# Optimization experiments

Measured on AMD Instinct MI355X. Metric: run time of the kernel, lower is better.

The kernel has to match this reference:

```python
import jax, jax.numpy as jnp
import numpy as np

INNER_DIM = 512
SCALE = 1.0 / np.sqrt(INNER_DIM).astype(np.float32)  # module scales by 1/sqrt(inner_dim), not head_dim


def setup_inputs() -> dict:
    key = jax.random.key(0)
    ks = jax.random.split(key, 7)
    b, n, d = 4, 4096, 512
    s = 0.02
    return {
        "x": jax.random.normal(ks[0], (b, n, d), jnp.float32),
        "y": jax.random.normal(ks[1], (b, n, d), jnp.float32),
        "Wq": jax.random.normal(ks[2], (INNER_DIM, d), jnp.float32) * s,  # torch Linear weight [out, in]
        "Wk": jax.random.normal(ks[3], (INNER_DIM, d), jnp.float32) * s,
        "Wv": jax.random.normal(ks[4], (INNER_DIM, d), jnp.float32) * s,
        "Wo": jax.random.normal(ks[5], (d, INNER_DIM), jnp.float32) * s,
        "bo": jax.random.normal(ks[6], (d,), jnp.float32) * s,
    }


def reference(x, y, Wq, Wk, Wv, Wo, bo):
    # q, k from x; v from y (bias-free projections)
    q = jnp.einsum('bnd,id->bni', x, Wq)
    k = jnp.einsum('bnd,id->bni', x, Wk)
    v = jnp.einsum('bnd,id->bni', y, Wv)
    # full [b, n, n] scores, scaled by 1/sqrt(inner_dim)
    alpha = jnp.einsum('bik,bjk->bij', q, k) * SCALE
    alpha = jax.nn.softmax(alpha, axis=-1)
    ctx = jnp.einsum('bij,bjd->bid', alpha, v)
    out = jnp.einsum('bid,od->bio', ctx, Wo) + bo
    return out
```

## Files before the change

kernel.cpp:

```cpp
#include <hip/hip_runtime.h>
#include <hip/hip_bf16.h>


typedef unsigned short u16;
typedef __bf16 bf16x8 __attribute__((ext_vector_type(8)));
typedef float f32x4 __attribute__((ext_vector_type(4)));

#define SCALE_QK 0.044194173824159216f

__device__ __forceinline__ u16 f2bf(float f) {
    __hip_bfloat16 h = __float2bfloat16(f);
    return __builtin_bit_cast(u16, h);
}

__device__ __forceinline__ void load_lds16(const void* g, void* l) {
    __builtin_amdgcn_global_load_lds(
        (const __attribute__((address_space(1))) void*)g,
        (__attribute__((address_space(3))) void*)l, 16, 0, 0);
}

__global__ void cvt_bf16_kernel(const float* __restrict__ src, u16* __restrict__ dst,
                                int n8, float scale) {
    int i = blockIdx.x * blockDim.x + threadIdx.x;
    if (i >= n8) return;
    const float4* s4 = (const float4*)src;
    float4 v0 = s4[2 * i], v1 = s4[2 * i + 1];
    union { u16 u[8]; uint4 v; } o;
    o.u[0] = f2bf(v0.x * scale); o.u[1] = f2bf(v0.y * scale);
    o.u[2] = f2bf(v0.z * scale); o.u[3] = f2bf(v0.w * scale);
    o.u[4] = f2bf(v1.x * scale); o.u[5] = f2bf(v1.y * scale);
    o.u[6] = f2bf(v1.z * scale); o.u[7] = f2bf(v1.w * scale);
    ((uint4*)dst)[i] = o.v;
}

__global__ void wvo_kernel(const float* __restrict__ Wo, const float* __restrict__ Wv,
                           float* __restrict__ Wvo) {
    int o = blockIdx.x, t = threadIdx.x;
    float a0 = 0.f, a1 = 0.f;
    for (int i = 0; i < 512; ++i) {
        float w = Wo[o * 512 + i];
        a0 += w * Wv[i * 512 + t];
        a1 += w * Wv[i * 512 + t + 256];
    }
    Wvo[o * 512 + t] = a0;
    Wvo[o * 512 + t + 256] = a1;
}

__launch_bounds__(512, 2)
__global__ void gemm256_exp_kernel(const u16* __restrict__ A, const u16* __restrict__ B,
                                   u16* __restrict__ Cout, int N, int lda, int ldb,
                                   long long sAz, long long sBz, long long sCz) {
    __shared__ u16 lds[8][8192];

    const int tid = threadIdx.x;
    const int wave = tid >> 6, lane = tid & 63;
    const int lr = lane & 15, lg = lane >> 4;
    const int wm = wave >> 2, wn = wave & 3;

    int bid = (blockIdx.z * gridDim.y + blockIdx.y) * gridDim.x + blockIdx.x;
    int lgc = (bid & 7) * 128 + (bid >> 3);
    const int bx = lgc & 15;
    int rem = lgc >> 4;
    const int by = rem & 15, z = rem >> 4;
    const int row0 = by * 256, col0 = bx * 256;

    const u16* Ab = A + (size_t)z * sAz;
    const u16* Bb = B + (size_t)z * sBz;

    const int rb = lane >> 2;
    const int kg8 = ((lane & 3) ^ (rb & 3)) << 3;

    f32x4 acc[8][4];
#pragma unroll
    for (int i = 0; i < 8; ++i)
#pragma unroll
        for (int j = 0; j < 4; ++j) acc[i][j] = (f32x4){0.f, 0.f, 0.f, 0.f};

#define STAGE_HALF(s_, slot_)                                                     \
    {                                                                             \
        const int h_ = (s_)&3, ts_ = (s_) >> 2;                                   \
        const u16* G_ = (h_ & 1) ? Bb : Ab;                                       \
        const int pan_ = (h_ & 1) ? col0 : row0;                                  \
        const int ld_ = (h_ & 1) ? ldb : lda;                                     \
        const int kofs_ = ts_ * 64 + (h_ >> 1) * 32 + kg8;                        \
        _Pragma("unroll") for (int j_ = 0; j_ < 2; ++j_) {                        \
            int r_ = (j_ * 8 + wave) * 16 + rb;                                   \
            load_lds16(G_ + (size_t)(pan_ + r_) * ld_ + kofs_,                    \
                       &lds[slot_][(j_ * 8 + wave) * 512]);                       \
        }                                                                         \
    }

    #pragma unroll
    for (int s = 0; s < 6; ++s) STAGE_HALF(s, s);
    asm volatile("s_waitcnt vmcnt(4)");
    __builtin_amdgcn_sched_barrier(0);
    __builtin_amdgcn_s_barrier();

    bf16x8 bfr[4];

#pragma unroll
    for (int i = 0; i < 4; ++i) {
#pragma unroll
        for (int p = 0; p < 8; ++p) {
            const int q = p & 3;
            const int ks = q >> 1;
            const int aslot = (p >> 2) * 4 + 2 * ks;
            const int bslot = aslot + 1;
            const int fmb = (q & 1) * 4;

            bf16x8 af[4];
#pragma unroll
            for (int f = 0; f < 4; ++f) {
                int row = wm * 128 + (fmb + f) * 16 + lr;
                af[f] = *(const bf16x8*)&lds[aslot][row * 32 + ((lg ^ (lr & 3)) << 3)];
            }
            if (q == 0 || q == 2) {
#pragma unroll
                for (int f = 0; f < 4; ++f) {
                    int row = wn * 64 + f * 16 + lr;
                    bfr[f] = *(const bf16x8*)&lds[bslot][row * 32 + ((lg ^ (lr & 3)) << 3)];
                }
            }

            {
                const int s = 8 * i + p + 6;
                if (s < 32) {
                    const int slot = (p + 6) & 7;
                    STAGE_HALF(s, slot);
                }
            }

            __builtin_amdgcn_sched_barrier(0);
            __builtin_amdgcn_s_barrier();
            asm volatile("s_waitcnt lgkmcnt(0)");
            __builtin_amdgcn_sched_barrier(0);

            __builtin_amdgcn_s_setprio(1);
#pragma unroll
            for (int f = 0; f < 4; ++f)
#pragma unroll
                for (int n = 0; n < 4; ++n)
                    acc[fmb + f][n] = __builtin_amdgcn_mfma_f32_16x16x32_bf16(
                        af[f], bfr[n], acc[fmb + f][n], 0, 0, 0);
            __builtin_amdgcn_s_setprio(0);

            if (p == 3) {
                if (i == 3) asm volatile("s_waitcnt vmcnt(0)");
                else        asm volatile("s_waitcnt vmcnt(4)");
            } else if (p == 7 && i < 3) {
                asm volatile("s_waitcnt vmcnt(4)");
            }
            __builtin_amdgcn_sched_barrier(0);
            __builtin_amdgcn_s_barrier();
        }
    }
#undef STAGE_HALF

    u16* C = Cout + (size_t)z * sCz;
#pragma unroll
    for (int fm = 0; fm < 8; ++fm)
#pragma unroll
        for (int fn = 0; fn < 4; ++fn)
#pragma unroll
            for (int reg = 0; reg < 4; ++reg) {
                int r = row0 + wm * 128 + fm * 16 + lg * 4 + reg;
                int c = col0 + wn * 64 + fn * 16 + lr;
                C[(size_t)r * N + c] = f2bf(__expf(acc[fm][fn][reg]));
            }
}

template <int EPI>
__launch_bounds__(256)
__global__ void gemm_bt_kernel(const u16* __restrict__ A, const u16* __restrict__ B,
                               void* __restrict__ Cout, int N, int K, int lda, int ldb,
                               long long sAz, long long sBz, long long sCz) {
    __shared__ u16 As[2][128 * 32];
    __shared__ u16 Bs[2][128 * 32];

    const int tid = threadIdx.x;
    const int wave = tid >> 6, lane = tid & 63;
    const int lr = lane & 15, lg = lane >> 4;
    const int wr = wave >> 1, wc = wave & 1;

    const int gx = gridDim.x, gy = gridDim.y;
    int bid = (blockIdx.z * gy + blockIdx.y) * gx + blockIdx.x;
    const int nwg = gx * gy * gridDim.z;
    int lgc = (bid & 7) * (nwg >> 3) + (bid >> 3);
    const int bx = lgc % gx;
    int rem = lgc / gx;
    const int by = rem % gy, z = rem / gy;
    const int row0 = by * 128, col0 = bx * 128;

    const u16* Ab = A + (size_t)z * sAz;
    const u16* Bb = B + (size_t)z * sBz;

    f32x4 acc[4][4];
#pragma unroll
    for (int i = 0; i < 4; ++i)
#pragma unroll
        for (int j = 0; j < 4; ++j) acc[i][j] = (f32x4){0.f, 0.f, 0.f, 0.f};

    const int KT = K >> 5;

#define STAGE(bufi, kt2)                                                          \
    {                                                                             \
        _Pragma("unroll") for (int i = 0; i < 2; ++i) {                           \
            int chunk = i * 256 + tid;                                            \
            int r = chunk >> 2, c4 = chunk & 3;                                   \
            load_lds16(Ab + (size_t)(row0 + r) * lda + (kt2) * 32 + c4 * 8,       \
                       &As[bufi][(i * 256 + wave * 64) * 8]);                     \
            load_lds16(Bb + (size_t)(col0 + r) * ldb + (kt2) * 32 + c4 * 8,       \
                       &Bs[bufi][(i * 256 + wave * 64) * 8]);                     \
        }                                                                         \
    }

    STAGE(0, 0);
    int buf = 0;
    for (int kt = 0; kt < KT; ++kt) {
        __syncthreads();
        if (kt + 1 < KT) STAGE(buf ^ 1, kt + 1);

        bf16x8 af[4], bfr[4];
#pragma unroll
        for (int mf = 0; mf < 4; ++mf)
            af[mf] = *(const bf16x8*)&As[buf][(wr * 64 + mf * 16 + lr) * 32 + lg * 8];
#pragma unroll
        for (int nf = 0; nf < 4; ++nf)
            bfr[nf] = *(const bf16x8*)&Bs[buf][(wc * 64 + nf * 16 + lr) * 32 + lg * 8];
#pragma unroll
        for (int mf = 0; mf < 4; ++mf)
#pragma unroll
            for (int nf = 0; nf < 4; ++nf)
                acc[mf][nf] = __builtin_amdgcn_mfma_f32_16x16x32_bf16(
                    af[mf], bfr[nf], acc[mf][nf], 0, 0, 0);
        buf ^= 1;
    }
#undef STAGE

    const int rbase = row0 + wr * 64;
    const int cbase = col0 + wc * 64;

    if (EPI == 0) {
        u16* C = (u16*)Cout + (size_t)z * sCz;
#pragma unroll
        for (int mf = 0; mf < 4; ++mf)
#pragma unroll
            for (int nf = 0; nf < 4; ++nf)
#pragma unroll
                for (int reg = 0; reg < 4; ++reg) {
                    int r = rbase + mf * 16 + lg * 4 + reg;
                    int c = cbase + nf * 16 + lr;
                    C[(size_t)r * N + c] = f2bf(acc[mf][nf][reg]);
                }
    } else {
        u16* C = (u16*)Cout;
#pragma unroll
        for (int mf = 0; mf < 4; ++mf)
#pragma unroll
            for (int nf = 0; nf < 4; ++nf) {
                int rg = rbase + mf * 16 + lg * 4;
                int bsel = rg >> 12, rl = rg & 4095;
                int c = cbase + nf * 16 + lr;
                union { u16 u[4]; uint2 v; } o;
#pragma unroll
                for (int reg = 0; reg < 4; ++reg) o.u[reg] = f2bf(acc[mf][nf][reg]);
                *(uint2*)(C + ((size_t)bsel << 21) + ((size_t)c << 12) + rl) = o.v;
            }
    }
}

__launch_bounds__(512, 4)
__global__ void pv_kernel(const u16* __restrict__ P, const u16* __restrict__ vwT,
                          float* __restrict__ part, float* __restrict__ lpart) {
    __shared__ u16 As[2][64 * 32];
    __shared__ u16 Bs[2][512 * 32];

    const int tid = threadIdx.x;
    const int wave = tid >> 6, lane = tid & 63;
    const int lr = lane & 15, lg = lane >> 4;

    int bid = blockIdx.x;
    int lgc = (bid & 7) * 64 + (bid >> 3);
    const int rp = lgc & 63;
    const int ks = (lgc >> 6) & 1;
    const int z = lgc >> 7;
    const int row0 = rp * 64;

    const u16* Pz = P + (size_t)z * 16777216 + (size_t)row0 * 4096 + ks * 2048;
    const u16* Vz = vwT + (size_t)z * 2097152 + ks * 2048;

    f32x4 acc[4][4];
#pragma unroll
    for (int i = 0; i < 4; ++i)
#pragma unroll
        for (int j = 0; j < 4; ++j) acc[i][j] = (f32x4){0.f, 0.f, 0.f, 0.f};
    float rs = 0.f;

#define STAGE(bufi, kt2)                                                          \
    {                                                                             \
        if (tid < 256) {                                                          \
            int r = tid >> 2, c4 = tid & 3;                                       \
            load_lds16(Pz + (size_t)r * 4096 + (kt2) * 32 + c4 * 8,               \
                       &As[bufi][wave * 512]);                                    \
        }                                                                         \
        _Pragma("unroll") for (int it = 0; it < 4; ++it) {                        \
            int c = it * 512 + tid;                                               \
            int r = c >> 2, c4 = c & 3;                                           \
            load_lds16(Vz + (size_t)r * 4096 + (kt2) * 32 + c4 * 8,               \
                       &Bs[bufi][(it * 512 + wave * 64) * 8]);                    \
        }                                                                         \
    }

    STAGE(0, 0);
    int buf = 0;
    for (int kt = 0; kt < 64; ++kt) {
        __syncthreads();
        if (kt + 1 < 64) STAGE(buf ^ 1, kt + 1);

        {
            uint2 rv = *(const uint2*)&As[buf][(tid >> 3) * 32 + (tid & 7) * 4];
            rs += __uint_as_float(rv.x << 16) + __uint_as_float(rv.x & 0xffff0000u) +
                  __uint_as_float(rv.y << 16) + __uint_as_float(rv.y & 0xffff0000u);
        }

        bf16x8 af[4];
#pragma unroll
        for (int mf = 0; mf < 4; ++mf)
            af[mf] = *(const bf16x8*)&As[buf][(mf * 16 + lr) * 32 + lg * 8];
#pragma unroll
        for (int nf = 0; nf < 4; ++nf) {
            bf16x8 bfr = *(const bf16x8*)&Bs[buf][(wave * 64 + nf * 16 + lr) * 32 + lg * 8];
#pragma unroll
            for (int mf = 0; mf < 4; ++mf)
                acc[mf][nf] = __builtin_amdgcn_mfma_f32_16x16x32_bf16(
                    af[mf], bfr, acc[mf][nf], 0, 0, 0);
        }
        buf ^= 1;
    }
#undef STAGE

    rs += __shfl_xor(rs, 1, 64);
    rs += __shfl_xor(rs, 2, 64);
    rs += __shfl_xor(rs, 4, 64);
    if ((tid & 7) == 0)
        lpart[(size_t)ks * 16384 + z * 4096 + row0 + (tid >> 3)] = rs;

    float* O = part + (size_t)ks * 8388608 + ((size_t)z * 4096 + row0) * 512;
#pragma unroll
    for (int mf = 0; mf < 4; ++mf)
#pragma unroll
        for (int nf = 0; nf < 4; ++nf) {
            int c = wave * 64 + nf * 16 + lr;
#pragma unroll
            for (int reg = 0; reg < 4; ++reg) {
                int r = mf * 16 + lg * 4 + reg;
                O[(size_t)r * 512 + c] = acc[mf][nf][reg];
            }
        }
}

__global__ void reduce_kernel(const float* __restrict__ part,
                              const float* __restrict__ lpart,
                              const float* __restrict__ bo,
                              float* __restrict__ out) {
    int i = blockIdx.x * blockDim.x + threadIdx.x;
    int r = i >> 7, c4 = i & 127;
    float inv = 1.0f / (lpart[r] + lpart[16384 + r]);
    float4 a = ((const float4*)part)[i];
    float4 b = ((const float4*)part)[i + 2097152];
    float4 bi = ((const float4*)bo)[c4];
    float4 o;
    o.x = (a.x + b.x) * inv + bi.x;
    o.y = (a.y + b.y) * inv + bi.y;
    o.z = (a.z + b.z) * inv + bi.z;
    o.w = (a.w + b.w) * inv + bi.w;
    ((float4*)out)[i] = o;
}

extern "C" void kernel_launch(void* const* d_in, const int* in_sizes, int n_in,
                              void* d_out, int out_size, void* d_ws, size_t ws_size,
                              hipStream_t stream) {
    const float* x  = (const float*)d_in[0];
    const float* y  = (const float*)d_in[1];
    const float* Wq = (const float*)d_in[2];
    const float* Wk = (const float*)d_in[3];
    const float* Wv = (const float*)d_in[4];
    const float* Wo = (const float*)d_in[5];
    const float* bo = (const float*)d_in[6];
    float* out = (float*)d_out;

    char* ws = (char*)d_ws;
    u16*   xb   = (u16*)(ws + 0);
    u16*   yb   = (u16*)(ws + 16777216);
    u16*   qk   = (u16*)(ws + 33554432);
    float* part = (float*)(ws + 0);
    u16*   vwT  = (u16*)(ws + 67108864);
    u16*   Wqkb = (u16*)(ws + 83886080);
    u16*   Wvob = (u16*)(ws + 84934656);
    float* Wvo  = (float*)(ws + 85458944);
    float* lpart= (float*)(ws + 86507520);
    u16*   P    = (u16*)(ws + 86638592);

    cvt_bf16_kernel<<<4096, 256, 0, stream>>>(x, xb, 1048576, 1.0f);
    cvt_bf16_kernel<<<4096, 256, 0, stream>>>(y, yb, 1048576, 1.0f);
    cvt_bf16_kernel<<<128, 256, 0, stream>>>(Wq, Wqkb, 32768, SCALE_QK);
    cvt_bf16_kernel<<<128, 256, 0, stream>>>(Wk, Wqkb + 262144, 32768, 1.0f);

    wvo_kernel<<<512, 256, 0, stream>>>(Wo, Wv, Wvo);
    cvt_bf16_kernel<<<128, 256, 0, stream>>>(Wvo, Wvob, 32768, 1.0f);

    gemm_bt_kernel<0><<<dim3(8, 128, 1), 256, 0, stream>>>(xb, Wqkb, qk,
                                                           1024, 512, 512, 512, 0, 0, 0);
    gemm_bt_kernel<1><<<dim3(4, 128, 1), 256, 0, stream>>>(yb, Wvob, vwT,
                                                           512, 512, 512, 512, 0, 0, 0);

    gemm256_exp_kernel<<<dim3(16, 16, 4), 512, 0, stream>>>(qk, qk + 512, P,
                                                            4096, 1024, 1024,
                                                            4194304, 4194304, 16777216);

    pv_kernel<<<512, 512, 0, stream>>>(P, vwT, part, lpart);

    reduce_kernel<<<8192, 256, 0, stream>>>(part, lpart, bo, out);
}
```

Measured before the change: 315.8 us.

## Retile PV GEMM to 256x256 pipeline, fuse fp32 conversion into projections

Replaces the 64-row PV kernel with a 256x256-tile kernel that uses a deep 8-slot LDS pipeline with swizzled layout, mirroring the QK kernel, so V tiles are reused across more rows. The projection GEMMs now read fp32 x/y directly and convert to bf16 in registers, which removes two full-size conversion passes. wvo_kernel computes four output rows per block so each Wv load is reused. The larger tiles reduce redundant global traffic but give fewer blocks and put more pressure on registers.

Result: slower. 334.2 us (+5.8%).

```diff
diff --git a/kernel.cpp b/kernel.cpp
--- a/kernel.cpp
+++ b/kernel.cpp
@@ -35,15 +35,22 @@
 
 __global__ void wvo_kernel(const float* __restrict__ Wo, const float* __restrict__ Wv,
                            float* __restrict__ Wvo) {
-    int o = blockIdx.x, t = threadIdx.x;
-    float a0 = 0.f, a1 = 0.f;
+    int ob = blockIdx.x * 4, t = threadIdx.x;
+    float a[4][2] = {{0.f, 0.f}, {0.f, 0.f}, {0.f, 0.f}, {0.f, 0.f}};
     for (int i = 0; i < 512; ++i) {
-        float w = Wo[o * 512 + i];
-        a0 += w * Wv[i * 512 + t];
-        a1 += w * Wv[i * 512 + t + 256];
-    }
-    Wvo[o * 512 + t] = a0;
-    Wvo[o * 512 + t + 256] = a1;
+        float v0 = Wv[i * 512 + t], v1 = Wv[i * 512 + t + 256];
+#pragma unroll
+        for (int r = 0; r < 4; ++r) {
+            float w = Wo[(ob + r) * 512 + i];
+            a[r][0] += w * v0;
+            a[r][1] += w * v1;
+        }
+    }
+#pragma unroll
+    for (int r = 0; r < 4; ++r) {
+        Wvo[(ob + r) * 512 + t] = a[r][0];
+        Wvo[(ob + r) * 512 + t + 256] = a[r][1];
+    }
 }
 
 __launch_bounds__(512, 2)
@@ -169,11 +176,158 @@
             }
 }
 
+__launch_bounds__(512, 2)
+__global__ void pv8_kernel(const u16* __restrict__ P, const u16* __restrict__ vwT,
+                           float* __restrict__ part, float* __restrict__ lpart) {
+    __shared__ u16 lds[8][8192];
+
+    const int tid = threadIdx.x;
+    const int wave = tid >> 6, lane = tid & 63;
+    const int lr = lane & 15, lg = lane >> 4;
+    const int wm = wave >> 2, wn = wave & 3;
+
+    int bid = blockIdx.x;
+    int lgc = (bid & 7) * 32 + (bid >> 3);
+    const int rp = lgc & 15;
+    const int t5 = lgc >> 4;
+    const int cx = t5 & 1, ks = (t5 >> 1) & 1, z = t5 >> 2;
+    const int row0 = rp * 256;
+    const int col0 = cx * 256;
+
+    const u16* Ab = P + (size_t)z * 16777216 + (size_t)ks * 2048;
+    const u16* Bb = vwT + (size_t)z * 2097152 + (size_t)ks * 2048;
+
+    const int rb = lane >> 2;
+    const int kg8 = ((lane & 3) ^ (rb & 3)) << 3;
+
+    f32x4 acc[8][4];
+#pragma unroll
+    for (int i = 0; i < 8; ++i)
+#pragma unroll
+        for (int j = 0; j < 4; ++j) acc[i][j] = (f32x4){0.f, 0.f, 0.f, 0.f};
+    float rsm[8] = {0.f, 0.f, 0.f, 0.f, 0.f, 0.f, 0.f, 0.f};
+
+#define STAGE_HALF(s_, slot_)                                                     \
+    {                                                                             \
+        const int h_ = (s_)&3, ts_ = (s_) >> 2;                                   \
+        const u16* G_ = (h_ & 1) ? Bb : Ab;                                       \
+        const int pan_ = (h_ & 1) ? col0 : row0;                                  \
+        const int kofs_ = ts_ * 64 + (h_ >> 1) * 32 + kg8;                        \
+        _Pragma("unroll") for (int j_ = 0; j_ < 2; ++j_) {                        \
+            int r_ = (j_ * 8 + wave) * 16 + rb;                                   \
+            load_lds16(G_ + (size_t)(pan_ + r_) * 4096 + kofs_,                   \
+                       &lds[slot_][(j_ * 8 + wave) * 512]);                       \
+        }                                                                         \
+    }
+
+    #pragma unroll
+    for (int s = 0; s < 6; ++s) STAGE_HALF(s, s);
+    asm volatile("s_waitcnt vmcnt(4)");
+    __builtin_amdgcn_sched_barrier(0);
+    __builtin_amdgcn_s_barrier();
+
+    bf16x8 bfr[4];
+
+    for (int i = 0; i < 16; ++i) {
+#pragma unroll
+        for (int p = 0; p < 8; ++p) {
+            const int q = p & 3;
+            const int ksl = q >> 1;
+            const int aslot = (p >> 2) * 4 + 2 * ksl;
+            const int bslot = aslot + 1;
+            const int fmb = (q & 1) * 4;
+
+            bf16x8 af[4];
+#pragma unroll
+            for (int f = 0; f < 4; ++f) {
+                int row = wm * 128 + (fmb + f) * 16 + lr;
+                af[f] = *(const bf16x8*)&lds[aslot][row * 32 + ((lg ^ (lr & 3)) << 3)];
+            }
+            if (q == 0 || q == 2) {
+#pragma unroll
+                for (int f = 0; f < 4; ++f) {
+                    int row = wn * 64 + f * 16 + lr;
+                    bfr[f] = *(const bf16x8*)&lds[bslot][row * 32 + ((lg ^ (lr & 3)) << 3)];
+                }
+            }
+
+            {
+                const int s = 8 * i + p + 6;
+                if (s < 128) {
+                    const int slot = (p + 6) & 7;
+                    STAGE_HALF(s, slot);
+                }
+            }
+
+            __builtin_amdgcn_sched_barrier(0);
+            __builtin_amdgcn_s_barrier();
+            asm volatile("s_waitcnt lgkmcnt(0)");
+            __builtin_amdgcn_sched_barrier(0);
+
+            __builtin_amdgcn_s_setprio(1);
+#pragma unroll
+            for (int f = 0; f < 4; ++f)
+#pragma unroll
+                for (int n = 0; n < 4; ++n)
+                    acc[fmb + f][n] = __builtin_amdgcn_mfma_f32_16x16x32_bf16(
+                        af[f], bfr[n], acc[fmb + f][n], 0, 0, 0);
+            __builtin_amdgcn_s_setprio(0);
+
+            if (wn == 0) {
+#pragma unroll
+                for (int f = 0; f < 4; ++f) {
+                    union { bf16x8 v; unsigned u[4]; } cv;
+                    cv.v = af[f];
+#pragma unroll
+                    for (int w = 0; w < 4; ++w)
+                        rsm[fmb + f] += __uint_as_float(cv.u[w] << 16) +
+                                        __uint_as_float(cv.u[w] & 0xffff0000u);
+                }
+            }
+
+            if (p == 3) {
+                if (i == 15) asm volatile("s_waitcnt vmcnt(0)");
+                else         asm volatile("s_waitcnt vmcnt(4)");
+            } else if (p == 7 && i < 15) {
+                asm volatile("s_waitcnt vmcnt(4)");
+            }
+            __builtin_amdgcn_sched_barrier(0);
+            __builtin_amdgcn_s_barrier();
+        }
+    }
+#undef STAGE_HALF
+
+    if (wn == 0) {
+#pragma unroll
+        for (int j = 0; j < 8; ++j) {
+            rsm[j] += __shfl_xor(rsm[j], 16, 64);
+            rsm[j] += __shfl_xor(rsm[j], 32, 64);
+        }
+        if (cx == 0 && lg == 0) {
+            float* lp = lpart + (size_t)ks * 16384 + z * 4096 + row0 + wm * 128;
+#pragma unroll
+            for (int j = 0; j < 8; ++j) lp[j * 16 + lr] = rsm[j];
+        }
+    }
+
+    float* O = part + (size_t)ks * 8388608 + ((size_t)z * 4096 + row0) * 512;
+#pragma unroll
+    for (int fm = 0; fm < 8; ++fm)
+#pragma unroll
+        for (int fn = 0; fn < 4; ++fn) {
+            int c = col0 + wn * 64 + fn * 16 + lr;
+#pragma unroll
+            for (int reg = 0; reg < 4; ++reg) {
+                int r = wm * 128 + fm * 16 + lg * 4 + reg;
+                O[(size_t)r * 512 + c] = acc[fm][fn][reg];
+            }
+        }
+}
+
 template <int EPI>
 __launch_bounds__(256)
-__global__ void gemm_bt_kernel(const u16* __restrict__ A, const u16* __restrict__ B,
-                               void* __restrict__ Cout, int N, int K, int lda, int ldb,
-                               long long sAz, long long sBz, long long sCz) {
+__global__ void gemm_f32a_kernel(const float* __restrict__ A, const u16* __restrict__ B,
+                                 void* __restrict__ Cout, int N, int K, int lda, int ldb) {
     __shared__ u16 As[2][128 * 32];
     __shared__ u16 Bs[2][128 * 32];
 
@@ -183,17 +337,12 @@
     const int wr = wave >> 1, wc = wave & 1;
 
     const int gx = gridDim.x, gy = gridDim.y;
-    int bid = (blockIdx.z * gy + blockIdx.y) * gx + blockIdx.x;
-    const int nwg = gx * gy * gridDim.z;
+    int bid = blockIdx.y * gx + blockIdx.x;
+    const int nwg = gx * gy;
     int lgc = (bid & 7) * (nwg >> 3) + (bid >> 3);
-    const int bx = lgc % gx;
-    int rem = lgc / gx;
-    const int by = rem % gy, z = rem / gy;
+    const int bx = lgc % gx, by = lgc / gx;
     const int row0 = by * 128, col0 = bx * 128;
 
-    const u16* Ab = A + (size_t)z * sAz;
-    const u16* Bb = B + (size_t)z * sBz;
-
     f32x4 acc[4][4];
 #pragma unroll
     for (int i = 0; i < 4; ++i)
@@ -201,24 +350,50 @@
         for (int j = 0; j < 4; ++j) acc[i][j] = (f32x4){0.f, 0.f, 0.f, 0.f};
 
     const int KT = K >> 5;
-
-#define STAGE(bufi, kt2)                                                          \
+    float4 ar[2][2];
+
+#define LOADA(kt2)                                                                \
     {                                                                             \
         _Pragma("unroll") for (int i = 0; i < 2; ++i) {                           \
             int chunk = i * 256 + tid;                                            \
             int r = chunk >> 2, c4 = chunk & 3;                                   \
-            load_lds16(Ab + (size_t)(row0 + r) * lda + (kt2) * 32 + c4 * 8,       \
-                       &As[bufi][(i * 256 + wave * 64) * 8]);                     \
-            load_lds16(Bb + (size_t)(col0 + r) * ldb + (kt2) * 32 + c4 * 8,       \
+            const float* src = A + (size_t)(row0 + r) * lda + (kt2) * 32 + c4 * 8;\
+            ar[i][0] = *(const float4*)src;                                       \
+            ar[i][1] = *(const float4*)(src + 4);                                 \
+        }                                                                         \
+    }
+#define WRITEA(bufi)                                                              \
+    {                                                                             \
+        _Pragma("unroll") for (int i = 0; i < 2; ++i) {                           \
+            int chunk = i * 256 + tid;                                            \
+            union { u16 u[8]; uint4 v; } cv;                                      \
+            const float* f = (const float*)&ar[i][0];                             \
+            _Pragma("unroll") for (int j = 0; j < 8; ++j) cv.u[j] = f2bf(f[j]);   \
+            *(uint4*)&As[bufi][chunk * 8] = cv.v;                                 \
+        }                                                                         \
+    }
+#define STAGEB(bufi, kt2)                                                         \
+    {                                                                             \
+        _Pragma("unroll") for (int i = 0; i < 2; ++i) {                           \
+            int chunk = i * 256 + tid;                                            \
+            int r = chunk >> 2, c4 = chunk & 3;                                   \
+            load_lds16(B + (size_t)(col0 + r) * ldb + (kt2) * 32 + c4 * 8,        \
                        &Bs[bufi][(i * 256 + wave * 64) * 8]);                     \
         }                                                                         \
     }
 
-    STAGE(0, 0);
+    LOADA(0);
+    WRITEA(0);
+    LOADA(1);
+    STAGEB(0, 0);
     int buf = 0;
     for (int kt = 0; kt < KT; ++kt) {
         __syncthreads();
-        if (kt + 1 < KT) STAGE(buf ^ 1, kt + 1);
+        if (kt + 1 < KT) {
+            WRITEA(buf ^ 1);
+            STAGEB(buf ^ 1, kt + 1);
+        }
+        if (kt + 2 < KT) LOADA(kt + 2);
 
         bf16x8 af[4], bfr[4];
 #pragma unroll
@@ -235,13 +410,15 @@
                     af[mf], bfr[nf], acc[mf][nf], 0, 0, 0);
         buf ^= 1;
     }
-#undef STAGE
+#undef LOADA
+#undef WRITEA
+#undef STAGEB
 
     const int rbase = row0 + wr * 64;
     const int cbase = col0 + wc * 64;
 
     if (EPI == 0) {
-        u16* C = (u16*)Cout + (size_t)z * sCz;
+        u16* C = (u16*)Cout;
 #pragma unroll
         for (int mf = 0; mf < 4; ++mf)
 #pragma unroll
@@ -267,96 +444,6 @@
                 *(uint2*)(C + ((size_t)bsel << 21) + ((size_t)c << 12) + rl) = o.v;
             }
     }
-}
-
-__launch_bounds__(512, 4)
-__global__ void pv_kernel(const u16* __restrict__ P, const u16* __restrict__ vwT,
-                          float* __restrict__ part, float* __restrict__ lpart) {
-    __shared__ u16 As[2][64 * 32];
-    __shared__ u16 Bs[2][512 * 32];
-
-    const int tid = threadIdx.x;
-    const int wave = tid >> 6, lane = tid & 63;
-    const int lr = lane & 15, lg = lane >> 4;
-
-    int bid = blockIdx.x;
-    int lgc = (bid & 7) * 64 + (bid >> 3);
-    const int rp = lgc & 63;
-    const int ks = (lgc >> 6) & 1;
-    const int z = lgc >> 7;
-    const int row0 = rp * 64;
-
-    const u16* Pz = P + (size_t)z * 16777216 + (size_t)row0 * 4096 + ks * 2048;
-    const u16* Vz = vwT + (size_t)z * 2097152 + ks * 2048;
-
-    f32x4 acc[4][4];
-#pragma unroll
-    for (int i = 0; i < 4; ++i)
-#pragma unroll
-        for (int j = 0; j < 4; ++j) acc[i][j] = (f32x4){0.f, 0.f, 0.f, 0.f};
-    float rs = 0.f;
-
-#define STAGE(bufi, kt2)                                                          \
-    {                                                                             \
-        if (tid < 256) {                                                          \
-            int r = tid >> 2, c4 = tid & 3;                                       \
-            load_lds16(Pz + (size_t)r * 4096 + (kt2) * 32 + c4 * 8,               \
-                       &As[bufi][wave * 512]);                                    \
-        }                                                                         \
-        _Pragma("unroll") for (int it = 0; it < 4; ++it) {                        \
-            int c = it * 512 + tid;                                               \
-            int r = c >> 2, c4 = c & 3;                                           \
-            load_lds16(Vz + (size_t)r * 4096 + (kt2) * 32 + c4 * 8,               \
-                       &Bs[bufi][(it * 512 + wave * 64) * 8]);                    \
-        }                                                                         \
-    }
-
-    STAGE(0, 0);
-    int buf = 0;
-    for (int kt = 0; kt < 64; ++kt) {
-        __syncthreads();
-        if (kt + 1 < 64) STAGE(buf ^ 1, kt + 1);
-
-        {
-            uint2 rv = *(const uint2*)&As[buf][(tid >> 3) * 32 + (tid & 7) * 4];
-            rs += __uint_as_float(rv.x << 16) + __uint_as_float(rv.x & 0xffff0000u) +
-                  __uint_as_float(rv.y << 16) + __uint_as_float(rv.y & 0xffff0000u);
-        }
-
-        bf16x8 af[4];
-#pragma unroll
-        for (int mf = 0; mf < 4; ++mf)
-            af[mf] = *(const bf16x8*)&As[buf][(mf * 16 + lr) * 32 + lg * 8];
-#pragma unroll
-        for (int nf = 0; nf < 4; ++nf) {
-            bf16x8 bfr = *(const bf16x8*)&Bs[buf][(wave * 64 + nf * 16 + lr) * 32 + lg * 8];
-#pragma unroll
-            for (int mf = 0; mf < 4; ++mf)
-                acc[mf][nf] = __builtin_amdgcn_mfma_f32_16x16x32_bf16(
-                    af[mf], bfr, acc[mf][nf], 0, 0, 0);
-        }
-        buf ^= 1;
-    }
-#undef STAGE
-
-    rs += __shfl_xor(rs, 1, 64);
-    rs += __shfl_xor(rs, 2, 64);
-    rs += __shfl_xor(rs, 4, 64);
-    if ((tid & 7) == 0)
-        lpart[(size_t)ks * 16384 + z * 4096 + row0 + (tid >> 3)] = rs;
-
-    float* O = part + (size_t)ks * 8388608 + ((size_t)z * 4096 + row0) * 512;
-#pragma unroll
-    for (int mf = 0; mf < 4; ++mf)
-#pragma unroll
-        for (int nf = 0; nf < 4; ++nf) {
-            int c = wave * 64 + nf * 16 + lr;
-#pragma unroll
-            for (int reg = 0; reg < 4; ++reg) {
-                int r = mf * 16 + lg * 4 + reg;
-                O[(size_t)r * 512 + c] = acc[mf][nf][reg];
-            }
-        }
 }
 
 __global__ void reduce_kernel(const float* __restrict__ part,
@@ -390,9 +477,7 @@
     float* out = (float*)d_out;
 
     char* ws = (char*)d_ws;
-    u16*   xb   = (u16*)(ws + 0);
-    u16*   yb   = (u16*)(ws + 16777216);
-    u16*   qk   = (u16*)(ws + 33554432);
+    u16*   qk   = (u16*)(ws + 0);
     float* part = (float*)(ws + 0);
     u16*   vwT  = (u16*)(ws + 67108864);
     u16*   Wqkb = (u16*)(ws + 83886080);
@@ -401,24 +486,19 @@
     float* lpart= (float*)(ws + 86507520);
     u16*   P    = (u16*)(ws + 86638592);
 
-    cvt_bf16_kernel<<<4096, 256, 0, stream>>>(x, xb, 1048576, 1.0f);
-    cvt_bf16_kernel<<<4096, 256, 0, stream>>>(y, yb, 1048576, 1.0f);
     cvt_bf16_kernel<<<128, 256, 0, stream>>>(Wq, Wqkb, 32768, SCALE_QK);
     cvt_bf16_kernel<<<128, 256, 0, stream>>>(Wk, Wqkb + 262144, 32768, 1.0f);
-
-    wvo_kernel<<<512, 256, 0, stream>>>(Wo, Wv, Wvo);
+    wvo_kernel<<<128, 256, 0, stream>>>(Wo, Wv, Wvo);
     cvt_bf16_kernel<<<128, 256, 0, stream>>>(Wvo, Wvob, 32768, 1.0f);
 
-    gemm_bt_kernel<0><<<dim3(8, 128, 1), 256, 0, stream>>>(xb, Wqkb, qk,
-                                                           1024, 512, 512, 512, 0, 0, 0);
-    gemm_bt_kernel<1><<<dim3(4, 128, 1), 256, 0, stream>>>(yb, Wvob, vwT,
-                                                           512, 512, 512, 512, 0, 0, 0);
+    gemm_f32a_kernel<0><<<dim3(8, 128), 256, 0, stream>>>(x, Wqkb, qk, 1024, 512, 512, 512);
+    gemm_f32a_kernel<1><<<dim3(4, 128), 256, 0, stream>>>(y, Wvob, vwT, 512, 512, 512, 512);
 
     gemm256_exp_kernel<<<dim3(16, 16, 4), 512, 0, stream>>>(qk, qk + 512, P,
                                                             4096, 1024, 1024,
                                                             4194304, 4194304, 16777216);
 
-    pv_kernel<<<512, 512, 0, stream>>>(P, vwT, part, lpart);
+    pv8_kernel<<<256, 512, 0, stream>>>(P, vwT, part, lpart);
 
     reduce_kernel<<<8192, 256, 0, stream>>>(part, lpart, bo, out);
 }
```
